# Kernel tuning notes

Measured on AMD Instinct MI355X. Metric: run time of the kernel, lower is better.

The kernel has to match this reference:

```python
import jax, jax.numpy as jnp
import numpy as np

NUM_HEADS = 12
NUM_GROUPS = 4
METRIC_SCALE = 1.0
CLS_MIX = 1.0
MEAN_MIX = 0.5
ROUTER_SCALE = 1.0
DIFF_SCALE = 1.0
B, N, D, HF = 16, 577, 768, 3072


def _ln(x, g, b, eps=1e-5):
    mu = jnp.mean(x, axis=-1, keepdims=True)
    var = jnp.mean(jnp.square(x - mu), axis=-1, keepdims=True)
    return (x - mu) * jax.lax.rsqrt(var + eps) * g + b


def setup_inputs() -> dict:
    key = jax.random.key(0)
    ks = iter(jax.random.split(key, 16))
    w = lambda shape, std: jax.random.normal(next(ks), shape, jnp.float32) * std
    return {
        "x": w((B, N, D), 1.0),
        "ln1_g": jnp.ones((D,)), "ln1_b": jnp.zeros((D,)),
        "ad_ln_g": jnp.ones((D,)), "ad_ln_b": jnp.zeros((D,)),
        "ad_w": w((D, D), 0.02),
        "w_qkv": w((D, 3 * D), 0.02),
        "w_proj": w((D, D), 0.02), "b_proj": jnp.zeros((D,)),
        "ln2_g": jnp.ones((D,)), "ln2_b": jnp.zeros((D,)),
        "fc1_w": w((D, HF), 0.02), "fc1_b": jnp.zeros((HF,)),
        "fc2_w": w((HF, D), 0.02), "fc2_b": jnp.zeros((D,)),
        "r_ln_g": jnp.ones((HF,)), "r_ln_b": jnp.zeros((HF,)),
        "r_proj_w": w((2 * HF, NUM_GROUPS), 0.02), "r_proj_b": jnp.zeros((NUM_GROUPS,)),
        "r_gate_w": w((2 * HF, 1), 0.02), "r_gate_b": jnp.full((1,), -2.0),
        "r_scale": jnp.full((NUM_GROUPS,), 0.1),
        "d_ln_g": jnp.ones((HF,)), "d_ln_b": jnp.zeros((HF,)),
        "d_out_w": w((HF, HF), 0.005),
        "d_gate_w": w((HF, 1), 0.02), "d_gate_b": jnp.full((1,), -1.5),
    }


def reference(x, ln1_g, ln1_b, ad_ln_g, ad_ln_b, ad_w, w_qkv, w_proj, b_proj,
              ln2_g, ln2_b, fc1_w, fc1_b, fc2_w, fc2_b,
              r_ln_g, r_ln_b, r_proj_w, r_proj_b, r_gate_w, r_gate_b, r_scale,
              d_ln_g, d_ln_b, d_out_w, d_gate_w, d_gate_b):
    b, n, d = x.shape
    hd = d // NUM_HEADS
    # ---- GeoAttention (pre-norm) ----
    h = _ln(x, ln1_g, ln1_b)
    # metric adapter: residual LN+Linear (SharedAttentionMetricAdapter)
    metric_h = h + METRIC_SCALE * (_ln(h, ad_ln_g, ad_ln_b) @ ad_w)
    # q,k from metric path; v from plain path (asymmetric Q/K vs V)
    qk = metric_h @ w_qkv[:, : 2 * d]                # [b,n,2d]
    v = h @ w_qkv[:, 2 * d :]                        # [b,n,d]
    q = qk[..., :d].reshape(b, n, NUM_HEADS, hd).transpose(0, 2, 1, 3)
    k = qk[..., d:].reshape(b, n, NUM_HEADS, hd).transpose(0, 2, 1, 3)
    v = v.reshape(b, n, NUM_HEADS, hd).transpose(0, 2, 1, 3)
    attn = jax.nn.softmax(jnp.einsum("bhnd,bhmd->bhnm", q, k) * (hd ** -0.5), axis=-1)
    out = jnp.einsum("bhnm,bhmd->bhnd", attn, v).transpose(0, 2, 1, 3).reshape(b, n, d)
    x = x + out @ w_proj + b_proj
    # ---- GeoMlp (pre-norm) ----
    h2 = _ln(x, ln2_g, ln2_b)
    hid = h2 @ fc1_w + fc1_b                         # [b,n,HF]
    # GroupCompetitionRouter on hidden
    rn = _ln(hid, r_ln_g, r_ln_b)
    summary = jnp.concatenate([CLS_MIX * rn[:, 0], MEAN_MIX * jnp.mean(rn[:, 1:], axis=1)], axis=-1)  # [b,2HF]
    wts = jax.nn.softmax(summary @ r_proj_w + r_proj_b, axis=-1)       # [b,G]
    gate = jax.nn.sigmoid(summary @ r_gate_w + r_gate_b)               # [b,1]
    centered = wts * float(NUM_GROUPS) - 1.0
    grouped = hid.reshape(b, n, NUM_GROUPS, HF // NUM_GROUPS)
    scale = 1.0 + ROUTER_SCALE * gate[:, None, :, None] * r_scale[None, None, :, None] * centered[:, None, :, None]
    hid = (grouped * scale).reshape(b, n, HF)
    # TokenDiffusionMixer on hidden
    dn = _ln(hid, d_ln_g, d_ln_b)
    tr = dn / jnp.maximum(jnp.linalg.norm(dn, axis=-1, keepdims=True), 1e-12)
    aff = jax.nn.softmax(jnp.einsum("bnc,bmc->bnm", tr, tr) * (HF ** -0.5), axis=-1)
    diffusion = jnp.einsum("bnm,bmc->bnc", aff, dn) - dn
    dgate = jax.nn.sigmoid(dn[:, 0] @ d_gate_w + d_gate_b)             # [b,1]
    hid = hid + DIFF_SCALE * dgate[:, :, None] * (diffusion @ d_out_w)
    # activation + fc2
    hid = jax.nn.gelu(hid, approximate=False)
    return x + hid @ fc2_w + fc2_b
```

## Files before the change

kernel.cpp:

```cpp
#include <hip/hip_runtime.h>
#include <math.h>

typedef unsigned short u16;
typedef unsigned int   u32;
typedef __attribute__((ext_vector_type(4))) float f32x4;
typedef __attribute__((ext_vector_type(4))) u32   u32x4;

#define DEV __device__ __forceinline__
#define AS1 __attribute__((address_space(1)))
#define AS3 __attribute__((address_space(3)))

DEV float b2f(u16 u){ u32 x = ((u32)u)<<16; float f; __builtin_memcpy(&f,&x,4); return f; }
DEV u16 f2b(float f){ u32 x; __builtin_memcpy(&x,&f,4); u32 r = x + 0x7FFFu + ((x>>16)&1u); return (u16)(r>>16); }

DEV float ldf(const float* p, long i){ return p[i]; }
DEV float ldf(const u16*   p, long i){ return b2f(p[i]); }

DEV void gload16(const u16* g, u16* l){
  __builtin_amdgcn_global_load_lds((const AS1 u32*)(const void*)g,
                                   (AS3 u32*)(void*)l, 16, 0, 0);
}

DEV float wave_sum(float v){
#pragma unroll
  for(int o=32;o;o>>=1) v += __shfl_down(v,o,64);
  return v;
}
DEV float wave_max(float v){
#pragma unroll
  for(int o=32;o;o>>=1) v = fmaxf(v, __shfl_down(v,o,64));
  return v;
}
DEV float block_sum(float v, float* tmp){
  v = wave_sum(v);
  if((threadIdx.x&63)==0) tmp[threadIdx.x>>6]=v;
  __syncthreads();
  float r = tmp[0]+tmp[1]+tmp[2]+tmp[3];
  __syncthreads();
  return r;
}
DEV float block_max(float v, float* tmp){
  v = wave_max(v);
  if((threadIdx.x&63)==0) tmp[threadIdx.x>>6]=v;
  __syncthreads();
  float r = fmaxf(fmaxf(tmp[0],tmp[1]),fmaxf(tmp[2],tmp[3]));
  __syncthreads();
  return r;
}

template<typename TI>
__global__ void transpose_pad(const TI* __restrict__ in, u16* __restrict__ out,
                              int R, int C, int Rpad, long strideI, long strideO){
  __shared__ u16 t[32][33];
  in  += (long)blockIdx.z*strideI;
  out += (long)blockIdx.z*strideO;
  int tx = threadIdx.x & 31, ty = threadIdx.x >> 5;
  int bc = blockIdx.x*32, br = blockIdx.y*32;
#pragma unroll
  for(int i=0;i<32;i+=8){
    int r = br+ty+i, c = bc+tx;
    float v = (r<R && c<C) ? ldf(in,(long)r*C+c) : 0.f;
    t[ty+i][tx] = f2b(v);
  }
  __syncthreads();
#pragma unroll
  for(int i=0;i<32;i+=8){
    int c = bc+ty+i, r = br+tx;
    if(c<C && r<Rpad) out[(long)c*Rpad + r] = t[tx][ty+i];
  }
}

template<typename TI>
__global__ void ln_rows(const TI* __restrict__ x, const float* __restrict__ g,
                        const float* __restrict__ b, u16* __restrict__ y, int W){
  __shared__ float tmp[4];
  long base=(long)blockIdx.x*W;
  float s=0.f, ss=0.f;
  for(int c=threadIdx.x;c<W;c+=256){ float v=ldf(x,base+c); s+=v; ss+=v*v; }
  s=block_sum(s,tmp); ss=block_sum(ss,tmp);
  float mu=s/W;
  float rstd=rsqrtf(fmaxf(ss/W-mu*mu,0.f)+1e-5f);
  for(int c=threadIdx.x;c<W;c+=256){
    float v=ldf(x,base+c);
    y[base+c]=f2b((v-mu)*rstd*g[c]+b[c]);
  }
}

__global__ void row_stats(const u16* __restrict__ x, float* __restrict__ stats, int W){
  __shared__ float tmp[4];
  long base=(long)blockIdx.x*W;
  float s=0.f,ss=0.f;
  for(int c=threadIdx.x;c<W;c+=256){ float v=b2f(x[base+c]); s+=v; ss+=v*v; }
  s=block_sum(s,tmp); ss=block_sum(ss,tmp);
  if(threadIdx.x==0){
    float mu=s/W;
    stats[2*(long)blockIdx.x]=mu;
    stats[2*(long)blockIdx.x+1]=rsqrtf(fmaxf(ss/W-mu*mu,0.f)+1e-5f);
  }
}

__global__ void dn_kernel(const u16* __restrict__ x, const float* __restrict__ g,
                          const float* __restrict__ b, u16* __restrict__ dn,
                          float* __restrict__ rn){
  const int W=3072;
  __shared__ float tmp[4];
  long base=(long)blockIdx.x*(long)W;
  float s=0.f,ss=0.f;
  for(int c=threadIdx.x;c<W;c+=256){ float v=b2f(x[base+c]); s+=v; ss+=v*v; }
  s=block_sum(s,tmp); ss=block_sum(ss,tmp);
  float mu=s/W;
  float rstd=rsqrtf(fmaxf(ss/W-mu*mu,0.f)+1e-5f);
  float sq=0.f;
  for(int c=threadIdx.x;c<W;c+=256){
    float v=(b2f(x[base+c])-mu)*rstd*g[c]+b[c];
    sq+=v*v;
  }
  sq=block_sum(sq,tmp);
  float r=1.f/fmaxf(sqrtf(sq),1e-12f);
  for(int c=threadIdx.x;c<W;c+=256){
    float v=(b2f(x[base+c])-mu)*rstd*g[c]+b[c];
    dn[base+c]=f2b(v);
  }
  if(threadIdx.x==0) rn[blockIdx.x]=r;
}

__global__ void softmax_rows(u16* __restrict__ S, int W, int Wp,
                             const float* __restrict__ rs, int rpb, float alpha){
  __shared__ float tmp[4];
  long row = blockIdx.x;
  u16* p = S + row*(long)Wp;
  float rowscale = alpha;
  const float* rsb = nullptr;
  if(rs){ long bt=row/rpb; int m=(int)(row%rpb); rsb = rs + bt*(long)rpb; rowscale *= rsb[m]; }
  float mx=-3e38f;
  for(int c=threadIdx.x;c<W;c+=256){
    float v=b2f(p[c])*rowscale; if(rs) v*=rsb[c];
    mx=fmaxf(mx,v);
  }
  mx=block_max(mx,tmp);
  float sm=0.f;
  for(int c=threadIdx.x;c<W;c+=256){
    float v=b2f(p[c])*rowscale; if(rs) v*=rsb[c];
    sm+=__expf(v-mx);
  }
  sm=block_sum(sm,tmp);
  float inv=1.f/sm;
  for(int c=threadIdx.x;c<W;c+=256){
    float v=b2f(p[c])*rowscale; if(rs) v*=rsb[c];
    p[c]=f2b(__expf(v-mx)*inv);
  }
  for(int c=W+threadIdx.x;c<Wp;c+=256) p[c]=0;
}

__global__ void split_heads(const u16* __restrict__ qk, u16* __restrict__ qh, u16* __restrict__ kh){
  int i = blockIdx.x*256+threadIdx.x;
  if(i >= 16*577*12*8) return;
  int dv = i&7; int h=(i>>3)%12; int bn=i/96;
  int b=bn/577, n=bn%577;
  long src=(long)bn*1536 + h*64 + dv*8;
  long dst=((long)((b*12+h)*577+n))*64 + dv*8;
  *(u32x4*)(qh+dst) = *(const u32x4*)(qk+src);
  *(u32x4*)(kh+dst) = *(const u32x4*)(qk+src+768);
}
__global__ void merge_heads(const u16* __restrict__ aoh, u16* __restrict__ aout){
  int i = blockIdx.x*256+threadIdx.x;
  if(i >= 16*577*12*8) return;
  int dv=i&7; int h=(i>>3)%12; int bn=i/96;
  int b=bn/577, n=bn%577;
  long dst=(long)bn*768 + h*64 + dv*8;
  long src=((long)((b*12+h)*577+n))*64 + dv*8;
  *(u32x4*)(aout+dst) = *(const u32x4*)(aoh+src);
}
__global__ void make_vT(const u16* __restrict__ v, u16* __restrict__ vT){
  long i = (long)blockIdx.x*256+threadIdx.x;
  if(i >= (long)192*64*608) return;
  int n=(int)(i%608); long q=i/608; int d=(int)(q&63); int bh=(int)(q>>6);
  int b=bh/12, h=bh%12;
  u16 val=0;
  if(n<577) val = v[((long)(b*577+n))*768 + h*64 + d];
  vT[i]=val;
}

__global__ void summary_kernel(const u16* __restrict__ hid, const float* __restrict__ stats,
                               const float* __restrict__ rg, const float* __restrict__ rb,
                               float* __restrict__ summ){
  int b=blockIdx.y;
  int c=blockIdx.x*256+threadIdx.x;
  const u16* hb=hid+(size_t)b*577*3072;
  const float* st=stats+(size_t)b*577*2;
  float g=rg[c], be=rb[c];
  float cls=(b2f(hb[c])-st[0])*st[1]*g+be;
  float acc=0.f;
  for(int n=1;n<577;n++) acc += (b2f(hb[(size_t)n*3072+c])-st[2*n])*st[2*n+1];
  summ[(size_t)b*6144+c]        = 1.0f*cls;
  summ[(size_t)b*6144+3072+c]   = 0.5f*(g*(acc*(1.f/576.f))+be);
}

__global__ void router_kernel(const float* __restrict__ summ, const float* __restrict__ pw,
                              const float* __restrict__ pb, const float* __restrict__ gw,
                              const float* __restrict__ gb, const float* __restrict__ rsc,
                              float* __restrict__ scalef){
  __shared__ float tmp[4];
  int b=blockIdx.x;
  float a0=0,a1=0,a2=0,a3=0,a4=0;
  for(int c=threadIdx.x;c<6144;c+=256){
    float sv=summ[(size_t)b*6144+c];
    a0+=sv*pw[c*4+0]; a1+=sv*pw[c*4+1]; a2+=sv*pw[c*4+2]; a3+=sv*pw[c*4+3];
    a4+=sv*gw[c];
  }
  a0=block_sum(a0,tmp); a1=block_sum(a1,tmp); a2=block_sum(a2,tmp);
  a3=block_sum(a3,tmp); a4=block_sum(a4,tmp);
  if(threadIdx.x==0){
    float l0=a0+pb[0], l1=a1+pb[1], l2=a2+pb[2], l3=a3+pb[3];
    float mx=fmaxf(fmaxf(l0,l1),fmaxf(l2,l3));
    float e0=__expf(l0-mx),e1=__expf(l1-mx),e2=__expf(l2-mx),e3=__expf(l3-mx);
    float s=e0+e1+e2+e3;
    float gate=1.f/(1.f+__expf(-(a4+gb[0])));
    float w0=e0/s,w1=e1/s,w2=e2/s,w3=e3/s;
    scalef[b*4+0]=1.f+gate*rsc[0]*(4.f*w0-1.f);
    scalef[b*4+1]=1.f+gate*rsc[1]*(4.f*w1-1.f);
    scalef[b*4+2]=1.f+gate*rsc[2]*(4.f*w2-1.f);
    scalef[b*4+3]=1.f+gate*rsc[3]*(4.f*w3-1.f);
  }
}

__global__ void scale_hid(u16* __restrict__ hid, const float* __restrict__ scalef){
  long i=(long)blockIdx.x*256+threadIdx.x;
  if(i >= (long)9232*3072/8) return;
  long e=i*8;
  int c=(int)(e%3072);
  int b=(int)((e/3072)/577);
  float sc=scalef[b*4 + c/768];
  u32x4 u = *(u32x4*)(hid+e);
  u16* pu=(u16*)&u;
#pragma unroll
  for(int j=0;j<8;j++) pu[j]=f2b(b2f(pu[j])*sc);
  *(u32x4*)(hid+e)=u;
}

__global__ void dgate_kernel(const u16* __restrict__ dn, const float* __restrict__ gw,
                             const float* __restrict__ gb, float* __restrict__ dgate){
  __shared__ float tmp[4];
  int b=blockIdx.x;
  const u16* row = dn + (size_t)b*577*3072;
  float a=0.f;
  for(int c=threadIdx.x;c<3072;c+=256) a+=b2f(row[c])*gw[c];
  a=block_sum(a,tmp);
  if(threadIdx.x==0) dgate[b]=1.f/(1.f+__expf(-(a+gb[0])));
}

constexpr int F_BIAS=1, F_RES=2, F_GELU=4, F_GATE=8, F_RESF32=16, F_OUTF32=32;

DEV int swz(int u){ int row=u>>2, sl=u&3; return row*4 + (sl ^ ((row>>1)&3)); }

template<int FLAGS>
__global__ __launch_bounds__(256,2) void gemm_bt(
  const u16* __restrict__ A, long lda, long szA,
  const u16* __restrict__ B, long ldb, long szB,
  void* __restrict__ Cv, long ldc, long szC,
  const float* __restrict__ bias,
  const void* __restrict__ resv, long ldr, long szR, float res_scale,
  const float* __restrict__ gate,
  float alpha, int M, int N, int K, int NX, int NY)
{
  __shared__ alignas(16) u16 shA[128*32];
  __shared__ alignas(16) u16 shB[128*32];
  const int nwg = (int)gridDim.x;
  const int orig = (int)blockIdx.x;
  const int q = nwg>>3, r = nwg&7;
  const int xcd = orig&7, idx = orig>>3;
  const int wg = (xcd<r ? xcd*(q+1) : r*(q+1)+(xcd-r)*q) + idx;
  const int bx = wg % NX; const int t_ = wg / NX;
  const int by = t_ % NY; const int z  = t_ / NY;

  A += (long)z*szA; B += (long)z*szB;
  const int tid=threadIdx.x, lane=tid&63, wid=tid>>6;
  const int wr=wid>>1, wc=wid&1;
  const long m0=(long)bx*128, n0=(long)by*128;
  f32x4 acc[4][4];
#pragma unroll
  for(int i=0;i<4;i++)
#pragma unroll
    for(int j=0;j<4;j++){ f32x4 zv={0.f,0.f,0.f,0.f}; acc[i][j]=zv; }

  const int lr = lane>>2, lsl = lane&3;
  const u16* pA[2]; const u16* pB[2]; u16* lA[2]; u16* lB[2];
#pragma unroll
  for(int i=0;i<2;i++){
    int ra = wid*32 + i*16 + lr;
    int kc = (lsl ^ ((ra>>1)&3))*8;
    long gr = m0+ra; if(gr>=M) gr=M-1;
    long gb = n0+ra; if(gb>=N) gb=N-1;
    pA[i] = A + gr*lda + kc;
    pB[i] = B + gb*ldb + kc;
    lA[i] = shA + (wid*32 + i*16)*32;
    lB[i] = shB + (wid*32 + i*16)*32;
  }

  for(int k0=0;k0<K;k0+=32){
    __syncthreads();
#pragma unroll
    for(int i=0;i<2;i++){
      gload16(pA[i]+k0, lA[i]);
      gload16(pB[i]+k0, lB[i]);
    }
    __syncthreads();
    const int ks = lane>>4, rr = lane&15;
    u32x4 av[4], bv[4];
#pragma unroll
    for(int mi=0;mi<4;mi++) av[mi] = ((const u32x4*)shA)[swz((wr*64+mi*16+rr)*4+ks)];
#pragma unroll
    for(int ni=0;ni<4;ni++) bv[ni] = ((const u32x4*)shB)[swz((wc*64+ni*16+rr)*4+ks)];
#pragma unroll
    for(int mi=0;mi<4;mi++)
#pragma unroll
      for(int ni=0;ni<4;ni++)
        asm volatile("v_mfma_f32_16x16x32_bf16 %0, %1, %2, %0"
                     : "+v"(acc[mi][ni]) : "v"(av[mi]), "v"(bv[ni]));
  }
  const float* resf = (const float*)resv + (long)z*szR;
  const u16*   resh = (const u16*)resv   + (long)z*szR;
  float* Cf = (float*)Cv + (long)z*szC;
  u16*   Ch = (u16*)Cv   + (long)z*szC;
  float gv = (FLAGS&F_GATE)? gate[z] : 1.f;
#pragma unroll
  for(int mi=0;mi<4;mi++){
#pragma unroll
    for(int ni=0;ni<4;ni++){
      long c0 = n0 + wc*64 + ni*16 + (lane&15);
      if(c0>=N) continue;
      float bb = (FLAGS&F_BIAS)? bias[c0] : 0.f;
#pragma unroll
      for(int r2=0;r2<4;r2++){
        long rw = m0 + wr*64 + mi*16 + (lane>>4)*4 + r2;
        if(rw>=M) continue;
        float t = acc[mi][ni][r2]*alpha*gv + bb;
        if(FLAGS&F_RES){
          float rvv = (FLAGS&F_RESF32)? resf[rw*ldr+c0] : b2f(resh[rw*ldr+c0]);
          t += res_scale*rvv;
        }
        if(FLAGS&F_GELU) t = 0.5f*t*(1.f+erff(t*0.70710678118654752f));
        if(FLAGS&F_OUTF32) Cf[rw*ldc+c0]=t;
        else               Ch[rw*ldc+c0]=f2b(t);
      }
    }
  }
}

static inline int gpack(int M,int N,int nb,int& NX,int& NY){
  NX=(M+127)/128; NY=(N+127)/128; return NX*NY*nb;
}

extern "C" void kernel_launch(void* const* d_in, const int* in_sizes, int n_in,
                              void* d_out, int out_size, void* d_ws, size_t ws_size,
                              hipStream_t stream){
  const int BNr=16*577;
  const float* x      = (const float*)d_in[0];
  const float* ln1_g  = (const float*)d_in[1];
  const float* ln1_b  = (const float*)d_in[2];
  const float* ad_ln_g= (const float*)d_in[3];
  const float* ad_ln_b= (const float*)d_in[4];
  const float* ad_w   = (const float*)d_in[5];
  const float* w_qkv  = (const float*)d_in[6];
  const float* w_proj = (const float*)d_in[7];
  const float* b_proj = (const float*)d_in[8];
  const float* ln2_g  = (const float*)d_in[9];
  const float* ln2_b  = (const float*)d_in[10];
  const float* fc1_w  = (const float*)d_in[11];
  const float* fc1_b  = (const float*)d_in[12];
  const float* fc2_w  = (const float*)d_in[13];
  const float* fc2_b  = (const float*)d_in[14];
  const float* r_ln_g = (const float*)d_in[15];
  const float* r_ln_b = (const float*)d_in[16];
  const float* r_proj_w=(const float*)d_in[17];
  const float* r_proj_b=(const float*)d_in[18];
  const float* r_gate_w=(const float*)d_in[19];
  const float* r_gate_b=(const float*)d_in[20];
  const float* r_scale =(const float*)d_in[21];
  const float* d_ln_g = (const float*)d_in[22];
  const float* d_ln_b = (const float*)d_in[23];
  const float* d_outw = (const float*)d_in[24];
  const float* d_gate_w=(const float*)d_in[25];
  const float* d_gate_b=(const float*)d_in[26];

  char* ws=(char*)d_ws;
  size_t off=0;
  auto take=[&](size_t nb){ size_t r=off; off=(off+nb+255)&~(size_t)255; return r; };
  auto al  =[&](size_t v){ return (v+255)&~(size_t)255; };
  const size_t o_qkvT = take((size_t)2304*768*2);
  const size_t o_adT  = take((size_t)768*768*2);
  const size_t o_projT= take((size_t)768*768*2);
  const size_t o_fc1T = take((size_t)3072*768*2);
  const size_t o_fc2T = take((size_t)768*3072*2);
  const size_t o_doutT= take((size_t)3072*3072*2);
  const size_t o_x2   = take((size_t)BNr*768*4);
  const size_t o_hid  = take((size_t)BNr*3072*2);
  const size_t o_stats= take((size_t)BNr*2*4);
  const size_t o_rn   = take((size_t)BNr*4);
  const size_t o_sum  = take((size_t)16*6144*4);
  const size_t o_scalef=take(64*4);
  const size_t o_dg   = take(64);
  const size_t o_h    = take((size_t)BNr*768*2);
  const size_t o_lnh  = take((size_t)BNr*768*2);
  const size_t o_metric=take((size_t)BNr*768*2);
  const size_t o_qk   = take((size_t)BNr*1536*2);
  const size_t o_v    = take((size_t)BNr*768*2);
  const size_t o_qh   = take((size_t)192*577*64*2);
  const size_t o_kh   = take((size_t)192*577*64*2);
  const size_t o_vT   = take((size_t)192*64*608*2);
  (void)o_v; (void)o_vT; (void)ws_size; (void)in_sizes; (void)n_in; (void)out_size;
  const size_t o_S    = o_qk;
  const size_t o_aoh  = o_metric;
  const size_t o_aout = o_h;
  const size_t o_h2   = o_lnh;
  const size_t o_dn   = o_h;
  const size_t o_aff  = al(o_dn + (size_t)BNr*3072*2);
  const size_t o_dnTb = al(o_aff + (size_t)16*577*608*2);
  const size_t o_diff = al(o_dnTb + (size_t)4*3072*608*2);
  const size_t o_hact = o_dn;

  u16* qkvT=(u16*)(ws+o_qkvT); u16* adT=(u16*)(ws+o_adT); u16* projT=(u16*)(ws+o_projT);
  u16* fc1T=(u16*)(ws+o_fc1T); u16* fc2T=(u16*)(ws+o_fc2T); u16* doutT=(u16*)(ws+o_doutT);
  float* x2=(float*)(ws+o_x2); u16* hid=(u16*)(ws+o_hid);
  float* stats=(float*)(ws+o_stats); float* rn=(float*)(ws+o_rn);
  float* summ=(float*)(ws+o_sum); float* scalef=(float*)(ws+o_scalef); float* dgate=(float*)(ws+o_dg);
  u16* hbuf=(u16*)(ws+o_h); u16* lnh=(u16*)(ws+o_lnh); u16* metric=(u16*)(ws+o_metric);
  u16* qkbuf=(u16*)(ws+o_qk); u16* vbuf=(u16*)(ws+o_v);
  u16* qh=(u16*)(ws+o_qh); u16* kh=(u16*)(ws+o_kh); u16* vT=(u16*)(ws+o_vT);
  u16* Sc=(u16*)(ws+o_S); u16* aoh=(u16*)(ws+o_aoh); u16* aout=(u16*)(ws+o_aout);
  u16* h2=(u16*)(ws+o_h2);
  u16* dn=(u16*)(ws+o_dn); u16* aff=(u16*)(ws+o_aff); u16* dnTb=(u16*)(ws+o_dnTb);
  u16* diff=(u16*)(ws+o_diff); u16* hact=(u16*)(ws+o_hact);

  dim3 blk(256);
  int NX, NY, ng;
  transpose_pad<float><<<dim3(72,24,1),blk,0,stream>>>(w_qkv, qkvT, 768,2304,768, 0,0);
  transpose_pad<float><<<dim3(24,24,1),blk,0,stream>>>(ad_w,  adT,  768,768, 768, 0,0);
  transpose_pad<float><<<dim3(24,24,1),blk,0,stream>>>(w_proj,projT,768,768, 768, 0,0);
  transpose_pad<float><<<dim3(96,24,1),blk,0,stream>>>(fc1_w, fc1T, 768,3072,768, 0,0);
  transpose_pad<float><<<dim3(24,96,1),blk,0,stream>>>(fc2_w, fc2T, 3072,768,3072,0,0);
  transpose_pad<float><<<dim3(96,96,1),blk,0,stream>>>(d_outw,doutT,3072,3072,3072,0,0);
  ln_rows<float><<<BNr,blk,0,stream>>>(x, ln1_g, ln1_b, hbuf, 768);
  ln_rows<u16>  <<<BNr,blk,0,stream>>>(hbuf, ad_ln_g, ad_ln_b, lnh, 768);
  ng=gpack(BNr,768,1,NX,NY);
  gemm_bt<F_RES><<<ng,blk,0,stream>>>(lnh,768,0, adT,768,0, metric,768,0,
      nullptr, hbuf,768,0, 1.f, nullptr, 1.f, BNr,768,768, NX,NY);
  ng=gpack(BNr,1536,1,NX,NY);
  gemm_bt<0><<<ng,blk,0,stream>>>(metric,768,0, qkvT,768,0, qkbuf,1536,0,
      nullptr, nullptr,0,0,0.f, nullptr, 1.f, BNr,1536,768, NX,NY);
  ng=gpack(BNr,768,1,NX,NY);
  gemm_bt<0><<<ng,blk,0,stream>>>(hbuf,768,0, qkvT+(size_t)1536*768,768,0, vbuf,768,0,
      nullptr, nullptr,0,0,0.f, nullptr, 1.f, BNr,768,768, NX,NY);
  split_heads<<<3462,blk,0,stream>>>(qkbuf, qh, kh);
  make_vT<<<29184,blk,0,stream>>>(vbuf, vT);
  for(int c=0;c<6;c++){
    const u16* qc=qh+(size_t)c*32*577*64;
    const u16* kc=kh+(size_t)c*32*577*64;
    ng=gpack(577,577,32,NX,NY);
    gemm_bt<0><<<ng,blk,0,stream>>>(qc,64,(long)577*64, kc,64,(long)577*64,
        Sc,608,(long)577*608, nullptr, nullptr,0,0,0.f, nullptr, 0.125f, 577,577,64, NX,NY);
    softmax_rows<<<32*577,blk,0,stream>>>(Sc,577,608, nullptr,577, 1.f);
    ng=gpack(577,64,32,NX,NY);
    gemm_bt<0><<<ng,blk,0,stream>>>(Sc,608,(long)577*608, vT+(size_t)c*32*64*608,608,(long)64*608,
        aoh+(size_t)c*32*577*64,64,(long)577*64, nullptr, nullptr,0,0,0.f, nullptr, 1.f, 577,64,608, NX,NY);
  }
  merge_heads<<<3462,blk,0,stream>>>(aoh, aout);
  ng=gpack(BNr,768,1,NX,NY);
  gemm_bt<F_RES|F_BIAS|F_RESF32|F_OUTF32><<<ng,blk,0,stream>>>(aout,768,0, projT,768,0,
      x2,768,0, b_proj, x,768,0, 1.f, nullptr, 1.f, BNr,768,768, NX,NY);
  ln_rows<float><<<BNr,blk,0,stream>>>(x2, ln2_g, ln2_b, h2, 768);
  ng=gpack(BNr,3072,1,NX,NY);
  gemm_bt<F_BIAS><<<ng,blk,0,stream>>>(h2,768,0, fc1T,768,0, hid,3072,0,
      fc1_b, nullptr,0,0,0.f, nullptr, 1.f, BNr,3072,768, NX,NY);
  row_stats<<<BNr,blk,0,stream>>>(hid, stats, 3072);
  summary_kernel<<<dim3(12,16),blk,0,stream>>>(hid, stats, r_ln_g, r_ln_b, summ);
  router_kernel<<<16,blk,0,stream>>>(summ, r_proj_w, r_proj_b, r_gate_w, r_gate_b, r_scale, scalef);
  scale_hid<<<13848,blk,0,stream>>>(hid, scalef);
  dn_kernel<<<BNr,blk,0,stream>>>(hid, d_ln_g, d_ln_b, dn, rn);
  dgate_kernel<<<16,blk,0,stream>>>(dn, d_gate_w, d_gate_b, dgate);
  ng=gpack(577,577,16,NX,NY);
  gemm_bt<0><<<ng,blk,0,stream>>>(dn,3072,(long)577*3072, dn,3072,(long)577*3072,
      aff,608,(long)577*608, nullptr, nullptr,0,0,0.f, nullptr, 1.f, 577,577,3072, NX,NY);
  softmax_rows<<<BNr,blk,0,stream>>>(aff,577,608, rn,577, 0.01804219634f);
  for(int g4=0; g4<4; ++g4){
    transpose_pad<u16><<<dim3(96,19,4),blk,0,stream>>>(dn+(size_t)g4*4*577*3072, dnTb,
        577,3072,608, (long)577*3072, (long)3072*608);
    ng=gpack(577,3072,4,NX,NY);
    gemm_bt<F_RES><<<ng,blk,0,stream>>>(aff+(size_t)g4*4*577*608,608,(long)577*608,
        dnTb,608,(long)3072*608, diff+(size_t)g4*4*577*3072,3072,(long)577*3072,
        nullptr, dn+(size_t)g4*4*577*3072,3072,(long)577*3072, -1.f, nullptr, 1.f, 577,3072,608, NX,NY);
  }
  ng=gpack(577,3072,16,NX,NY);
  gemm_bt<F_RES|F_GATE|F_GELU><<<ng,blk,0,stream>>>(diff,3072,(long)577*3072,
      doutT,3072,0, hact,3072,(long)577*3072, nullptr, hid,3072,(long)577*3072, 1.f,
      dgate, 1.f, 577,3072,3072, NX,NY);
  ng=gpack(BNr,768,1,NX,NY);
  gemm_bt<F_RES|F_BIAS|F_RESF32|F_OUTF32><<<ng,blk,0,stream>>>(hact,3072,0,
      fc2T,3072,0, d_out,768,0, fc2_b, x2,768,0, 1.f, nullptr, 1.f, BNr,768,3072, NX,NY);
}
```

Before: 1.553 ms.

## Add 256x256 tile GEMM for large GEMMs and fold router scaling into consumers

Adds a 512-thread GEMM kernel with 256x256 output tiles, double-buffered LDS staging via direct global-to-LDS loads and MFMA priority hints. It replaces the 128x128 GEMM for the QK projection, fc1 and the big d_out GEMM, which now runs as one flat batch over all rows. The separate scale_hid pass is removed: dn_kernel applies the router scale while loading rows into LDS, and the d_out GEMM epilogue applies it to the residual. Larger tiles raise data reuse per block but use more LDS and registers and give fewer blocks; hid is left unscaled, so any other consumer of it must now scale it too.

After: 1.522 ms. 2.0% less time.

```diff
diff --git a/kernel.cpp b/kernel.cpp
--- a/kernel.cpp
+++ b/kernel.cpp
@@ -100,25 +100,33 @@
 }
 
 __global__ void dn_kernel(const u16* __restrict__ x, const float* __restrict__ g,
-                          const float* __restrict__ b, u16* __restrict__ dn,
-                          float* __restrict__ rn){
+                          const float* __restrict__ b, const float* __restrict__ scalef,
+                          u16* __restrict__ dn, float* __restrict__ rn){
   const int W=3072;
   __shared__ float tmp[4];
-  long base=(long)blockIdx.x*(long)W;
+  __shared__ u16 rowb[3072];
+  long row=(long)blockIdx.x;
+  long base=row*(long)W;
+  int bz=(int)(row/577);
   float s=0.f,ss=0.f;
-  for(int c=threadIdx.x;c<W;c+=256){ float v=b2f(x[base+c]); s+=v; ss+=v*v; }
+  for(int c=threadIdx.x;c<W;c+=256){
+    float sc=scalef[bz*4 + ((c>>8)/3)];
+    float v=b2f(x[base+c])*sc;
+    rowb[c]=f2b(v);
+    s+=v; ss+=v*v;
+  }
   s=block_sum(s,tmp); ss=block_sum(ss,tmp);
   float mu=s/W;
   float rstd=rsqrtf(fmaxf(ss/W-mu*mu,0.f)+1e-5f);
   float sq=0.f;
   for(int c=threadIdx.x;c<W;c+=256){
-    float v=(b2f(x[base+c])-mu)*rstd*g[c]+b[c];
+    float v=(b2f(rowb[c])-mu)*rstd*g[c]+b[c];
     sq+=v*v;
   }
   sq=block_sum(sq,tmp);
   float r=1.f/fmaxf(sqrtf(sq),1e-12f);
   for(int c=threadIdx.x;c<W;c+=256){
-    float v=(b2f(x[base+c])-mu)*rstd*g[c]+b[c];
+    float v=(b2f(rowb[c])-mu)*rstd*g[c]+b[c];
     dn[base+c]=f2b(v);
   }
   if(threadIdx.x==0) rn[blockIdx.x]=r;
@@ -224,20 +232,6 @@
   }
 }
 
-__global__ void scale_hid(u16* __restrict__ hid, const float* __restrict__ scalef){
-  long i=(long)blockIdx.x*256+threadIdx.x;
-  if(i >= (long)9232*3072/8) return;
-  long e=i*8;
-  int c=(int)(e%3072);
-  int b=(int)((e/3072)/577);
-  float sc=scalef[b*4 + c/768];
-  u32x4 u = *(u32x4*)(hid+e);
-  u16* pu=(u16*)&u;
-#pragma unroll
-  for(int j=0;j<8;j++) pu[j]=f2b(b2f(pu[j])*sc);
-  *(u32x4*)(hid+e)=u;
-}
-
 __global__ void dgate_kernel(const u16* __restrict__ dn, const float* __restrict__ gw,
                              const float* __restrict__ gb, float* __restrict__ dgate){
   __shared__ float tmp[4];
@@ -249,7 +243,7 @@
   if(threadIdx.x==0) dgate[b]=1.f/(1.f+__expf(-(a+gb[0])));
 }
 
-constexpr int F_BIAS=1, F_RES=2, F_GELU=4, F_GATE=8, F_RESF32=16, F_OUTF32=32;
+constexpr int F_BIAS=1, F_RES=2, F_GELU=4, F_GATE=8, F_RESF32=16, F_OUTF32=32, F_SCRES=64;
 
 DEV int swz(int u){ int row=u>>2, sl=u&3; return row*4 + (sl ^ ((row>>1)&3)); }
 
@@ -349,6 +343,146 @@
 
 static inline int gpack(int M,int N,int nb,int& NX,int& NY){
   NX=(M+127)/128; NY=(N+127)/128; return NX*NY*nb;
+}
+
+template<int FLAGS>
+__global__ __launch_bounds__(512,2) void gemm256(
+  const u16* __restrict__ A, long lda,
+  const u16* __restrict__ B, long ldb,
+  u16* __restrict__ C, long ldc,
+  const float* __restrict__ bias,
+  const u16* __restrict__ res, long ldr,
+  const float* __restrict__ gate, const float* __restrict__ scres,
+  float irpz, float alpha, int M, int N, int K, int NX)
+{
+  __shared__ u16 smem[65536];
+  const int nwg=(int)gridDim.x, orig=(int)blockIdx.x;
+  const int qq=nwg>>3, rr8=nwg&7, xcd=orig&7, idx=orig>>3;
+  const int wg=(xcd<rr8? xcd*(qq+1): rr8*(qq+1)+(xcd-rr8)*qq)+idx;
+  const int bx=wg%NX, by=wg/NX;
+  const long m0=(long)bx*256, n0=(long)by*256;
+  const int tid=threadIdx.x, lane=tid&63, wid=tid>>6;
+  const int wr=wid>>2, wc=wid&3;
+
+  f32x4 acc[8][4];
+#pragma unroll
+  for(int i=0;i<8;i++)
+#pragma unroll
+    for(int j=0;j<4;j++){ f32x4 zv={0.f,0.f,0.f,0.f}; acc[i][j]=zv; }
+
+  const u16* sA[2][2]; const u16* sB[2][2];
+#pragma unroll
+  for(int kh=0;kh<2;kh++)
+#pragma unroll
+    for(int jj=0;jj<2;jj++){
+      int s=jj*512+tid, row=s>>2, sl=(s&3)^((s>>3)&3);
+      long ar=m0+row; if(ar>=M) ar=M-1;
+      long br=n0+row; if(br>=N) br=N-1;
+      sA[kh][jj]=A+ar*lda+kh*32+sl*8;
+      sB[kh][jj]=B+br*ldb+kh*32+sl*8;
+    }
+  const int dst0=(wid*64)*8, dst1=(512+wid*64)*8;
+  const int ks=lane>>4, l15=lane&15;
+  const int phys=(ks^((l15>>1)&3))*8;
+  const int aBase=(wr*128+l15)*32+phys;
+  const int bBase=(wc*64 +l15)*32+phys;
+  const int NT=K>>6;
+
+#define STG(t,c,kh) { long k0_=(long)(t)*64; \
+    gload16(sA[kh][0]+k0_, smem + (c)*16384 + (kh)*8192 + dst0); \
+    gload16(sA[kh][1]+k0_, smem + (c)*16384 + (kh)*8192 + dst1); \
+    gload16(sB[kh][0]+k0_, smem + 32768 + (c)*16384 + (kh)*8192 + dst0); \
+    gload16(sB[kh][1]+k0_, smem + 32768 + (c)*16384 + (kh)*8192 + dst1); }
+
+  STG(0,0,0); STG(0,0,1);
+  asm volatile("s_waitcnt vmcnt(4)" ::: "memory");
+  __builtin_amdgcn_s_barrier();
+  asm volatile("" ::: "memory");
+
+  u32x4 av[4], bv[4];
+  for(int t=0;t<NT;++t){
+    const int cur=t&1, nxt=cur^1;
+    const u16* sa=smem + cur*16384;
+    const u16* sb=smem + 32768 + cur*16384;
+    const bool pf=(t+1<NT);
+    if(pf) STG(t+1,nxt,0);
+#pragma unroll
+    for(int j=0;j<4;j++) bv[j]=*(const u32x4*)(sb + bBase + j*512);
+#pragma unroll
+    for(int i=0;i<4;i++) av[i]=*(const u32x4*)(sa + aBase + i*512);
+    __builtin_amdgcn_s_setprio(1);
+#pragma unroll
+    for(int i=0;i<4;i++)
+#pragma unroll
+      for(int j=0;j<4;j++)
+        asm volatile("v_mfma_f32_16x16x32_bf16 %0, %1, %2, %0":"+v"(acc[i][j]):"v"(av[i]),"v"(bv[j]));
+    __builtin_amdgcn_s_setprio(0);
+#pragma unroll
+    for(int i=0;i<4;i++) av[i]=*(const u32x4*)(sa + aBase + 2048 + i*512);
+    __builtin_amdgcn_s_setprio(1);
+#pragma unroll
+    for(int i=0;i<4;i++)
+#pragma unroll
+      for(int j=0;j<4;j++)
+        asm volatile("v_mfma_f32_16x16x32_bf16 %0, %1, %2, %0":"+v"(acc[4+i][j]):"v"(av[i]),"v"(bv[j]));
+    __builtin_amdgcn_s_setprio(0);
+    if(pf) asm volatile("s_waitcnt vmcnt(4)" ::: "memory");
+    else   asm volatile("s_waitcnt vmcnt(0)" ::: "memory");
+    __builtin_amdgcn_s_barrier();
+    asm volatile("" ::: "memory");
+    if(pf) STG(t+1,nxt,1);
+#pragma unroll
+    for(int j=0;j<4;j++) bv[j]=*(const u32x4*)(sb + 8192 + bBase + j*512);
+#pragma unroll
+    for(int i=0;i<4;i++) av[i]=*(const u32x4*)(sa + 8192 + aBase + i*512);
+    __builtin_amdgcn_s_setprio(1);
+#pragma unroll
+    for(int i=0;i<4;i++)
+#pragma unroll
+      for(int j=0;j<4;j++)
+        asm volatile("v_mfma_f32_16x16x32_bf16 %0, %1, %2, %0":"+v"(acc[i][j]):"v"(av[i]),"v"(bv[j]));
+    __builtin_amdgcn_s_setprio(0);
+#pragma unroll
+    for(int i=0;i<4;i++) av[i]=*(const u32x4*)(sa + 8192 + aBase + 2048 + i*512);
+    __builtin_amdgcn_s_setprio(1);
+#pragma unroll
+    for(int i=0;i<4;i++)
+#pragma unroll
+      for(int j=0;j<4;j++)
+        asm volatile("v_mfma_f32_16x16x32_bf16 %0, %1, %2, %0":"+v"(acc[4+i][j]):"v"(av[i]),"v"(bv[j]));
+    __builtin_amdgcn_s_setprio(0);
+    if(pf) asm volatile("s_waitcnt vmcnt(4)" ::: "memory");
+    else   asm volatile("s_waitcnt vmcnt(0)" ::: "memory");
+    __builtin_amdgcn_s_barrier();
+    asm volatile("" ::: "memory");
+  }
+#undef STG
+
+#pragma unroll
+  for(int mf=0;mf<8;mf++){
+#pragma unroll
+    for(int j=0;j<4;j++){
+      long c0 = n0 + wc*64 + j*16 + l15;
+      float bb=(FLAGS&F_BIAS)? bias[c0]:0.f;
+      int cg=((int)(c0>>8))/3;
+#pragma unroll
+      for(int r2=0;r2<4;r2++){
+        long rw = m0 + wr*128 + mf*16 + ks*4 + r2;
+        if(rw>=M) continue;
+        float t=acc[mf][j][r2]*alpha;
+        if(FLAGS&(F_GATE|F_SCRES)){
+          int z=(int)(((float)rw+0.5f)*irpz);
+          if(FLAGS&F_GATE) t*=gate[z];
+          if(FLAGS&F_SCRES) t += scres[z*4+cg]*b2f(res[rw*ldr+c0]);
+        } else if(FLAGS&F_RES){
+          t += b2f(res[rw*ldr+c0]);
+        }
+        t+=bb;
+        if(FLAGS&F_GELU) t=0.5f*t*(1.f+erff(t*0.70710678118654752f));
+        C[rw*ldc+c0]=f2b(t);
+      }
+    }
+  }
 }
 
 extern "C" void kernel_launch(void* const* d_in, const int* in_sizes, int n_in,
@@ -432,7 +566,7 @@
   u16* dn=(u16*)(ws+o_dn); u16* aff=(u16*)(ws+o_aff); u16* dnTb=(u16*)(ws+o_dnTb);
   u16* diff=(u16*)(ws+o_diff); u16* hact=(u16*)(ws+o_hact);
 
-  dim3 blk(256);
+  dim3 blk(256), blk5(512);
   int NX, NY, ng;
   transpose_pad<float><<<dim3(72,24,1),blk,0,stream>>>(w_qkv, qkvT, 768,2304,768, 0,0);
   transpose_pad<float><<<dim3(24,24,1),blk,0,stream>>>(ad_w,  adT,  768,768, 768, 0,0);
@@ -445,9 +579,8 @@
   ng=gpack(BNr,768,1,NX,NY);
   gemm_bt<F_RES><<<ng,blk,0,stream>>>(lnh,768,0, adT,768,0, metric,768,0,
       nullptr, hbuf,768,0, 1.f, nullptr, 1.f, BNr,768,768, NX,NY);
-  ng=gpack(BNr,1536,1,NX,NY);
-  gemm_bt<0><<<ng,blk,0,stream>>>(metric,768,0, qkvT,768,0, qkbuf,1536,0,
-      nullptr, nullptr,0,0,0.f, nullptr, 1.f, BNr,1536,768, NX,NY);
+  gemm256<0><<<dim3(37*6),blk5,0,stream>>>(metric,768, qkvT,768, qkbuf,1536,
+      nullptr, nullptr,0, nullptr,nullptr, 0.f, 1.f, BNr,1536,768, 37);
   ng=gpack(BNr,768,1,NX,NY);
   gemm_bt<0><<<ng,blk,0,stream>>>(hbuf,768,0, qkvT+(size_t)1536*768,768,0, vbuf,768,0,
       nullptr, nullptr,0,0,0.f, nullptr, 1.f, BNr,768,768, NX,NY);
@@ -469,14 +602,12 @@
   gemm_bt<F_RES|F_BIAS|F_RESF32|F_OUTF32><<<ng,blk,0,stream>>>(aout,768,0, projT,768,0,
       x2,768,0, b_proj, x,768,0, 1.f, nullptr, 1.f, BNr,768,768, NX,NY);
   ln_rows<float><<<BNr,blk,0,stream>>>(x2, ln2_g, ln2_b, h2, 768);
-  ng=gpack(BNr,3072,1,NX,NY);
-  gemm_bt<F_BIAS><<<ng,blk,0,stream>>>(h2,768,0, fc1T,768,0, hid,3072,0,
-      fc1_b, nullptr,0,0,0.f, nullptr, 1.f, BNr,3072,768, NX,NY);
+  gemm256<F_BIAS><<<dim3(37*12),blk5,0,stream>>>(h2,768, fc1T,768, hid,3072,
+      fc1_b, nullptr,0, nullptr,nullptr, 0.f, 1.f, BNr,3072,768, 37);
   row_stats<<<BNr,blk,0,stream>>>(hid, stats, 3072);
   summary_kernel<<<dim3(12,16),blk,0,stream>>>(hid, stats, r_ln_g, r_ln_b, summ);
   router_kernel<<<16,blk,0,stream>>>(summ, r_proj_w, r_proj_b, r_gate_w, r_gate_b, r_scale, scalef);
-  scale_hid<<<13848,blk,0,stream>>>(hid, scalef);
-  dn_kernel<<<BNr,blk,0,stream>>>(hid, d_ln_g, d_ln_b, dn, rn);
+  dn_kernel<<<BNr,blk,0,stream>>>(hid, d_ln_g, d_ln_b, scalef, dn, rn);
   dgate_kernel<<<16,blk,0,stream>>>(dn, d_gate_w, d_gate_b, dgate);
   ng=gpack(577,577,16,NX,NY);
   gemm_bt<0><<<ng,blk,0,stream>>>(dn,3072,(long)577*3072, dn,3072,(long)577*3072,
@@ -490,10 +621,8 @@
         dnTb,608,(long)3072*608, diff+(size_t)g4*4*577*3072,3072,(long)577*3072,
         nullptr, dn+(size_t)g4*4*577*3072,3072,(long)577*3072, -1.f, nullptr, 1.f, 577,3072,608, NX,NY);
   }
-  ng=gpack(577,3072,16,NX,NY);
-  gemm_bt<F_RES|F_GATE|F_GELU><<<ng,blk,0,stream>>>(diff,3072,(long)577*3072,
-      doutT,3072,0, hact,3072,(long)577*3072, nullptr, hid,3072,(long)577*3072, 1.f,
-      dgate, 1.f, 577,3072,3072, NX,NY);
+  gemm256<F_GELU|F_GATE|F_SCRES><<<dim3(37*12),blk5,0,stream>>>(diff,3072, doutT,3072,
+      hact,3072, nullptr, hid,3072, dgate, scalef, 1.f/577.f, 1.f, BNr,3072,3072, 37);
   ng=gpack(BNr,768,1,NX,NY);
   gemm_bt<F_RES|F_BIAS|F_RESF32|F_OUTF32><<<ng,blk,0,stream>>>(hact,3072,0,
       fc2T,3072,0, d_out,768,0, fc2_b, x2,768,0, 1.f, nullptr, 1.f, BNr,768,3072, NX,NY);
```
